# Optimization experiments

Hardware: AMD Instinct MI355X
Metric: run time of the kernel (lower is better)

## Reference

```python
import jax, jax.numpy as jnp
import numpy as np

EPS = 1e-05
B, M, N, P = 32, 1024, 1024, 256


def _xavier(key, shape):
    fan_in, fan_out = shape[0], shape[1]
    limit = np.sqrt(6.0 / (fan_in + fan_out))
    return jax.random.uniform(key, shape, jnp.float32, -limit, limit)


def setup_inputs() -> dict:
    key = jax.random.key(0)
    ks = jax.random.split(key, 6)
    return {
        "x": jax.random.normal(ks[0], (B, M, N), jnp.float32),
        "original_xj_y": _xavier(ks[1], (N, P)),
        "original_xi_y": _xavier(ks[2], (M, P)),
        "permuted_xj_y": _xavier(ks[3], (M, P)),
        "permuted_xi_y": _xavier(ks[4], (N, P)),
        "gamma_o_sum": jnp.ones((P,), jnp.float32),
        "gamma_o": jnp.ones((P, P), jnp.float32),
        "gamma_p_sum": jnp.ones((P,), jnp.float32),
        "gamma_p": jnp.ones((P, P), jnp.float32),
        "gamma": jnp.ones((P, P), jnp.float32),
        "beta_o_sum": jnp.zeros((P,), jnp.float32),
        "beta_o": jnp.zeros((P, P), jnp.float32),
        "beta_p_sum": jnp.zeros((P,), jnp.float32),
        "beta_p": jnp.zeros((P, P), jnp.float32),
        "beta": jnp.zeros((P, P), jnp.float32),
    }


def _normalize(x, axes, gamma, beta):
    mean = jnp.mean(x, axis=axes, keepdims=True)
    std = jnp.sqrt(jnp.var(x, axis=axes, keepdims=True, ddof=1))  # torch std is unbiased
    return gamma * ((x - mean) / (std + EPS)) + beta


def reference(x, original_xj_y, original_xi_y, permuted_xj_y, permuted_xi_y,
              gamma_o_sum, gamma_o, gamma_p_sum, gamma_p, gamma,
              beta_o_sum, beta_o, beta_p_sum, beta_p, beta):
    permuted = jnp.swapaxes(x, -1, -2)  # [B, N, M]

    # original path
    oyy = x @ original_xj_y                      # [B, M, P]
    o_sum = _normalize(oyy.sum(axis=-2), (-1,), gamma_o_sum, beta_o_sum) + 1.0  # [B, P]
    oyy = jnp.swapaxes(oyy, -1, -2) @ original_xi_y  # [B, P, P]
    oyy = jnp.swapaxes(oyy, -1, -2)
    oyy = _normalize(oyy, (-2, -1), gamma_o, beta_o)

    # permuted path
    pyy = permuted @ permuted_xj_y               # [B, N, P]
    p_sum = _normalize(pyy.sum(axis=-2), (-1,), gamma_p_sum, beta_p_sum) + 1.0  # [B, P]
    pyy = jnp.swapaxes(pyy, -1, -2) @ permuted_xi_y  # [B, P, P]
    pyy = jnp.swapaxes(pyy, -1, -2)
    pyy = _normalize(pyy, (-2, -1), gamma_p, beta_p)

    relations = jnp.einsum('ij,ik->ijk', o_sum, p_sum)  # [B, P, P]
    projected = (oyy * relations) @ (pyy * relations)   # [B, P, P]
    projected = _normalize(projected, (-2, -1), gamma, beta)
    return (projected, relations)
```

## Files before the change

### kernel.cpp

```cpp
#include <hip/hip_runtime.h>
#include <hip/hip_bf16.h>

#define PP 256
#define BB 32
#define MM 1024
#define NN 1024

constexpr float EPSF = 1e-5f;

typedef __attribute__((ext_vector_type(8))) short short8v;
typedef __attribute__((ext_vector_type(4))) short short4v;
typedef __attribute__((ext_vector_type(4))) float f32x4;

__device__ inline float bf2f(short s) {
  union { unsigned u; float f; } cv;
  cv.u = ((unsigned)(unsigned short)s) << 16;
  return cv.f;
}
__device__ inline short f2bf(float f) {
  union { float f; unsigned u; } cv; cv.f = f;
  unsigned u = cv.u;
  unsigned r = (u + 0x7fffu + ((u >> 16) & 1u)) >> 16;
  return (short)r;
}

__device__ inline void gload16(const void* g, void* l) {
  __builtin_amdgcn_global_load_lds(
      (const __attribute__((address_space(1))) unsigned*)g,
      (__attribute__((address_space(3))) unsigned*)l, 16, 0, 0);
}

__global__ __launch_bounds__(256)
void wconv4(const float* __restrict__ s0, const float* __restrict__ s1,
            const float* __restrict__ s2, const float* __restrict__ s3,
            short* __restrict__ d0, short* __restrict__ d1,
            short* __restrict__ d2, short* __restrict__ d3)
{
  const float* src = (blockIdx.z == 0) ? s0 : (blockIdx.z == 1) ? s1
                    : (blockIdx.z == 2) ? s2 : s3;
  short* dst = (blockIdx.z == 0) ? d0 : (blockIdx.z == 1) ? d1
              : (blockIdx.z == 2) ? d2 : d3;
  __shared__ float tile[64][65];
  const int c0 = blockIdx.x * 64, r0 = blockIdx.y * 64;
  const int tid = threadIdx.x;
#pragma unroll
  for (int i = 0; i < 16; ++i) {
    int idx = i * 256 + tid;
    int r = idx >> 6, c = idx & 63;
    tile[r][c] = src[(long)(r0 + r) * 256 + (c0 + c)];
  }
  __syncthreads();
#pragma unroll
  for (int i = 0; i < 16; ++i) {
    int idx = i * 256 + tid;
    int rr = idx >> 6, cc = idx & 63;
    dst[(long)(c0 + rr) * 1024 + (r0 + cc)] = f2bf(tile[cc][rr]);
  }
}

__global__ __launch_bounds__(256)
void tr2_f32(const float* __restrict__ s0, const float* __restrict__ s1,
             float* __restrict__ d0, float* __restrict__ d1)
{
  const float* src = blockIdx.z ? s1 : s0;
  float* dst = blockIdx.z ? d1 : d0;
  __shared__ float tile[64][65];
  const int c0 = blockIdx.x * 64, r0 = blockIdx.y * 64;
  const int tid = threadIdx.x;
#pragma unroll
  for (int i = 0; i < 16; ++i) {
    int idx = i * 256 + tid;
    int r = idx >> 6, c = idx & 63;
    tile[r][c] = src[(long)(r0 + r) * 256 + (c0 + c)];
  }
  __syncthreads();
#pragma unroll
  for (int i = 0; i < 16; ++i) {
    int idx = i * 256 + tid;
    int rr = idx >> 6, cc = idx & 63;
    dst[(long)(c0 + rr) * 256 + (r0 + cc)] = tile[cc][rr];
  }
}

__global__ __launch_bounds__(256, 4)
void gemm_xcat(const float* __restrict__ x, const short* __restrict__ wcat,
               short* __restrict__ oyyT, short* __restrict__ UT,
               float* __restrict__ rowsum)
{
  constexpr int BM = 128, BN = 128;
  __shared__ short As[2][4 * BM * 8];
  __shared__ short Bs[2][4 * BN * 8];

  const int b = blockIdx.z;
  const float* Ab = x + (long)b * MM * NN;
  const int m0 = blockIdx.x * BM;
  const int n0 = blockIdx.y * BN;

  const int tid = threadIdx.x;
  const int l = tid & 63, w = tid >> 6;
  const int wr = w >> 1, wc = w & 1;
  const int lk = l >> 4, lr = l & 15;
  const int sm = tid >> 2, skc = tid & 3;

  const float* aptr0 = Ab + (long)(m0 + sm) * NN + skc * 8;
  const float* aptr1 = Ab + (long)(m0 + 64 + sm) * NN + skc * 8;
  const int bn = tid & 127, bk0 = (tid >> 7) * 8;
  const short* bptr = wcat + (long)(n0 + bn) * NN + bk0;

  const int sA0 = ((skc * BM + sm) * 8) ^ (skc << 4);
  const int sA1 = ((skc * BM + 64 + sm) * 8) ^ (skc << 4);

  f32x4 acc[4][4];
#pragma unroll
  for (int fm = 0; fm < 4; ++fm)
#pragma unroll
    for (int fn = 0; fn < 4; ++fn)
      acc[fm][fn] = (f32x4){0.f, 0.f, 0.f, 0.f};

  float rs0 = 0.f, rs1 = 0.f;
  const bool doRs = (blockIdx.y == 0);
  float4 a00, a01, a10, a11;

#define XCAT_LOAD_A(k0_) do { \
    a00 = *reinterpret_cast<const float4*>(aptr0 + (k0_)); \
    a01 = *reinterpret_cast<const float4*>(aptr0 + (k0_) + 4); \
    a10 = *reinterpret_cast<const float4*>(aptr1 + (k0_)); \
    a11 = *reinterpret_cast<const float4*>(aptr1 + (k0_) + 4); \
  } while (0)

#define XCAT_STAGE_B(buf_, k0_) do { \
    gload16(bptr + (k0_), &Bs[buf_][tid * 8]); \
    gload16(bptr + (k0_) + 16, &Bs[buf_][(tid + 256) * 8]); \
  } while (0)

#define XCAT_STAGE_A(buf_) do { \
    if (doRs) { \
      rs0 += a00.x + a00.y + a00.z + a00.w + a01.x + a01.y + a01.z + a01.w; \
      rs1 += a10.x + a10.y + a10.z + a10.w + a11.x + a11.y + a11.z + a11.w; \
    } \
    short8v pk0, pk1; \
    pk0[0] = f2bf(a00.x); pk0[1] = f2bf(a00.y); pk0[2] = f2bf(a00.z); pk0[3] = f2bf(a00.w); \
    pk0[4] = f2bf(a01.x); pk0[5] = f2bf(a01.y); pk0[6] = f2bf(a01.z); pk0[7] = f2bf(a01.w); \
    pk1[0] = f2bf(a10.x); pk1[1] = f2bf(a10.y); pk1[2] = f2bf(a10.z); pk1[3] = f2bf(a10.w); \
    pk1[4] = f2bf(a11.x); pk1[5] = f2bf(a11.y); pk1[6] = f2bf(a11.z); pk1[7] = f2bf(a11.w); \
    *reinterpret_cast<short8v*>(&As[buf_][sA0]) = pk0; \
    *reinterpret_cast<short8v*>(&As[buf_][sA1]) = pk1; \
  } while (0)

  XCAT_LOAD_A(0);
  XCAT_STAGE_B(0, 0);
  XCAT_STAGE_A(0);
  __syncthreads();

  for (int kt = 0; kt < 32; ++kt) {
    const int cur = kt & 1, nxt = cur ^ 1;
    if (kt < 31) {
      const int k1 = (kt + 1) * 32;
      XCAT_LOAD_A(k1);
      XCAT_STAGE_B(nxt, k1);
    }
    short8v af[4], bf[4];
#pragma unroll
    for (int fm = 0; fm < 4; ++fm) {
      const int row = wr * 64 + fm * 16 + lr;
      af[fm] = *reinterpret_cast<const short8v*>(&As[cur][((lk * BM + row) * 8) ^ (lk << 4)]);
    }
#pragma unroll
    for (int fn = 0; fn < 4; ++fn)
      bf[fn] = *reinterpret_cast<const short8v*>(&Bs[cur][(lk * BN + wc * 64 + fn * 16 + lr) * 8]);
#pragma unroll
    for (int fm = 0; fm < 4; ++fm)
#pragma unroll
      for (int fn = 0; fn < 4; ++fn)
        acc[fm][fn] = __builtin_amdgcn_mfma_f32_16x16x32_bf16(
            af[fm], bf[fn], acc[fm][fn], 0, 0, 0);
    if (kt < 31) XCAT_STAGE_A(nxt);
    __syncthreads();
  }

  if (doRs) {
    rs0 += __shfl_xor(rs0, 1); rs0 += __shfl_xor(rs0, 2);
    rs1 += __shfl_xor(rs1, 1); rs1 += __shfl_xor(rs1, 2);
    if ((tid & 3) == 0) {
      rowsum[(long)b * MM + m0 + sm] = rs0;
      rowsum[(long)b * MM + m0 + 64 + sm] = rs1;
    }
  }

  short* Cb = ((n0 < 256) ? oyyT : UT) + (long)b * PP * MM;
  const int nb = n0 & 255;
#pragma unroll
  for (int fm = 0; fm < 4; ++fm)
#pragma unroll
    for (int fn = 0; fn < 4; ++fn) {
      const int c = nb + wc * 64 + fn * 16 + lr;
      const int rb = m0 + wr * 64 + fm * 16 + lk * 4;
      short4v pk;
#pragma unroll
      for (int j = 0; j < 4; ++j) pk[j] = f2bf(acc[fm][fn][j]);
      *reinterpret_cast<short4v*>(&Cb[(long)c * MM + rb]) = pk;
    }
}

__global__ __launch_bounds__(256)
void gemm_dual(const short* __restrict__ oyyT, const short* __restrict__ wo2T,
               const short* __restrict__ UT, const short* __restrict__ wp1T,
               float* __restrict__ t2T, float* __restrict__ p2)
{
  constexpr int BM = 64, BN = 64;
  __shared__ short As[2][4 * BM * 8];
  __shared__ short Bs[2][4 * BN * 8];

  const int z = blockIdx.z;
  const short* Ab; const short* Bb; float* Cb;
  if (z < 32) { Ab = oyyT + (long)z * PP * MM; Bb = wo2T; Cb = t2T + ((long)z << 16); }
  else { Ab = UT + (long)(z - 32) * PP * MM; Bb = wp1T; Cb = p2 + ((long)(z - 32) << 16); }

  const int m0 = blockIdx.x * BM, n0 = blockIdx.y * BN;
  const int tid = threadIdx.x;
  const int l = tid & 63, w = tid >> 6;
  const int wr = w >> 1, wc = w & 1;
  const int lk = l >> 4, lr = l & 15;
  const int kc = tid >> 6, mloc = tid & 63;
  const short* aP = Ab + (long)(m0 + mloc) * MM + kc * 8;
  const short* bP = Bb + (long)(n0 + mloc) * MM + kc * 8;

  f32x4 acc[2][2];
#pragma unroll
  for (int fm = 0; fm < 2; ++fm)
#pragma unroll
    for (int fn = 0; fn < 2; ++fn)
      acc[fm][fn] = (f32x4){0.f, 0.f, 0.f, 0.f};

  gload16(aP, &As[0][tid * 8]);
  gload16(bP, &Bs[0][tid * 8]);
  __syncthreads();

  for (int kt = 0; kt < 32; ++kt) {
    const int cur = kt & 1, nxt = cur ^ 1;
    if (kt < 31) {
      gload16(aP + (kt + 1) * 32, &As[nxt][tid * 8]);
      gload16(bP + (kt + 1) * 32, &Bs[nxt][tid * 8]);
    }
    short8v af[2], bf[2];
#pragma unroll
    for (int fm = 0; fm < 2; ++fm)
      af[fm] = *(const short8v*)&As[cur][(lk * BM + wr * 32 + fm * 16 + lr) * 8];
#pragma unroll
    for (int fn = 0; fn < 2; ++fn)
      bf[fn] = *(const short8v*)&Bs[cur][(lk * BN + wc * 32 + fn * 16 + lr) * 8];
#pragma unroll
    for (int fm = 0; fm < 2; ++fm)
#pragma unroll
      for (int fn = 0; fn < 2; ++fn)
        acc[fm][fn] = __builtin_amdgcn_mfma_f32_16x16x32_bf16(
            af[fm], bf[fn], acc[fm][fn], 0, 0, 0);
    __syncthreads();
  }

#pragma unroll
  for (int fm = 0; fm < 2; ++fm)
#pragma unroll
    for (int fn = 0; fn < 2; ++fn) {
      const int c = n0 + wc * 32 + fn * 16 + lr;
      const int rb = m0 + wr * 32 + fm * 16 + lk * 4;
      *(f32x4*)&Cb[(long)c * PP + rb] = acc[fm][fn];
    }
}

__global__ __launch_bounds__(256)
void gemm_pp(const short* __restrict__ A, const short* __restrict__ BT,
             float* __restrict__ C)
{
  constexpr int BM = 64, BN = 64;
  __shared__ short As[2][4 * BM * 8];
  __shared__ short Bs[2][4 * BN * 8];
  const int b = blockIdx.z;
  const short* Ab = A + ((long)b << 16);
  const short* Bb = BT + ((long)b << 16);
  float* Cb = C + ((long)b << 16);
  const int m0 = blockIdx.x * BM, n0 = blockIdx.y * BN;
  const int tid = threadIdx.x;
  const int l = tid & 63, w = tid >> 6;
  const int wr = w >> 1, wc = w & 1;
  const int lk = l >> 4, lr = l & 15;
  const int kc = tid >> 6, mloc = tid & 63;
  const short* aP = Ab + (long)(m0 + mloc) * PP + kc * 8;
  const short* bP = Bb + (long)(n0 + mloc) * PP + kc * 8;

  f32x4 acc[2][2];
#pragma unroll
  for (int fm = 0; fm < 2; ++fm)
#pragma unroll
    for (int fn = 0; fn < 2; ++fn)
      acc[fm][fn] = (f32x4){0.f, 0.f, 0.f, 0.f};

  gload16(aP, &As[0][tid * 8]);
  gload16(bP, &Bs[0][tid * 8]);
  __syncthreads();

  for (int kt = 0; kt < 8; ++kt) {
    const int cur = kt & 1, nxt = cur ^ 1;
    if (kt < 7) {
      gload16(aP + (kt + 1) * 32, &As[nxt][tid * 8]);
      gload16(bP + (kt + 1) * 32, &Bs[nxt][tid * 8]);
    }
    short8v af[2], bf[2];
#pragma unroll
    for (int fm = 0; fm < 2; ++fm)
      af[fm] = *(const short8v*)&As[cur][(lk * BM + wr * 32 + fm * 16 + lr) * 8];
#pragma unroll
    for (int fn = 0; fn < 2; ++fn)
      bf[fn] = *(const short8v*)&Bs[cur][(lk * BN + wc * 32 + fn * 16 + lr) * 8];
#pragma unroll
    for (int fm = 0; fm < 2; ++fm)
#pragma unroll
      for (int fn = 0; fn < 2; ++fn)
        acc[fm][fn] = __builtin_amdgcn_mfma_f32_16x16x32_bf16(
            af[fm], bf[fn], acc[fm][fn], 0, 0, 0);
    __syncthreads();
  }

#pragma unroll
  for (int fm = 0; fm < 2; ++fm)
#pragma unroll
    for (int fn = 0; fn < 2; ++fn) {
      const int c = n0 + wc * 32 + fn * 16 + lr;
      const int rb = m0 + wr * 32 + fm * 16 + lk * 4;
#pragma unroll
      for (int j = 0; j < 4; ++j)
        Cb[(long)(rb + j) * PP + c] = acc[fm][fn][j];
    }
}

__global__ __launch_bounds__(256)
void colsum_bf16(const short* __restrict__ srcT, float* __restrict__ raw)
{
  const int b = blockIdx.y;
  const int w = threadIdx.x >> 6, l = threadIdx.x & 63;
  const int p = blockIdx.x * 4 + w;
  const short* row = srcT + ((long)b * 256 + p) * 1024;
  short8v v1 = *(const short8v*)&row[l * 8];
  short8v v2 = *(const short8v*)&row[(64 + l) * 8];
  float s = 0.f;
#pragma unroll
  for (int j = 0; j < 8; ++j) s += bf2f(v1[j]) + bf2f(v2[j]);
#pragma unroll
  for (int off = 32; off; off >>= 1) s += __shfl_down(s, off);
  if (l == 0) raw[(long)b * 256 + p] = s;
}

__global__ __launch_bounds__(256)
void psum_dot(const short* __restrict__ wp1T, const float* __restrict__ rowsum,
              float* __restrict__ rawP)
{
  __shared__ float rsm[1024];
  const int b = blockIdx.x;
  for (int i = threadIdx.x; i < 1024; i += 256) rsm[i] = rowsum[(long)b * 1024 + i];
  __syncthreads();
  const int p = threadIdx.x;
  const short* wrow = wp1T + (long)p * 1024;
  float s = 0.f;
  for (int k = 0; k < 1024; k += 8) {
    short8v v = *(const short8v*)&wrow[k];
#pragma unroll
    for (int j = 0; j < 8; ++j) s = fmaf(bf2f(v[j]), rsm[k + j], s);
  }
  rawP[(long)b * 256 + p] = s;
}

__device__ inline void block_reduce2(float& v1, float& v2, float* red)
{
#pragma unroll
  for (int off = 32; off > 0; off >>= 1) {
    v1 += __shfl_down(v1, off);
    v2 += __shfl_down(v2, off);
  }
  const int lane = threadIdx.x & 63, wid = threadIdx.x >> 6;
  if (lane == 0) { red[wid * 2] = v1; red[wid * 2 + 1] = v2; }
  __syncthreads();
  v1 = red[0] + red[2] + red[4] + red[6];
  v2 = red[1] + red[3] + red[5] + red[7];
}

__global__ __launch_bounds__(256)
void norm_sum2(const float* __restrict__ raw2,
               const float* __restrict__ g_os, const float* __restrict__ b_os,
               const float* __restrict__ g_ps, const float* __restrict__ b_ps,
               float* __restrict__ o_sum, float* __restrict__ p_sum)
{
  const int bb = blockIdx.x;
  const bool isP = bb >= 32;
  const int b = bb & 31;
  const float* raw = raw2 + (isP ? 8192 : 0);
  const float* gamma = isP ? g_ps : g_os;
  const float* beta = isP ? b_ps : b_os;
  float* outp = isP ? p_sum : o_sum;
  const int p = threadIdx.x;
  float s = raw[(long)b * 256 + p];
  __shared__ float red[8];
  float v1 = s, v2 = s * s;
  block_reduce2(v1, v2, red);
  const float mean = v1 / 256.0f;
  float var = fmaxf((v2 - v1 * mean) / 255.0f, 0.f);
  const float inv = 1.0f / (sqrtf(var) + EPSF);
  outp[(long)b * 256 + p] = gamma[p] * (s - mean) * inv + beta[p] + 1.0f;
}

__global__ __launch_bounds__(256)
void stats_dual(const float* __restrict__ t2T, const float* __restrict__ p2,
                float* __restrict__ part)
{
  const int y = blockIdx.y, chunk = blockIdx.x;
  const float* s = (y < 32 ? t2T + ((long)y << 16)
                           : p2 + ((long)(y - 32) << 16)) + (long)chunk * 8192;
  float v1 = 0.f, v2 = 0.f;
  for (int i = threadIdx.x; i < 2048; i += 256) {
    float4 xv = *reinterpret_cast<const float4*>(&s[i * 4]);
    v1 += xv.x + xv.y + xv.z + xv.w;
    v2 = fmaf(xv.x, xv.x, fmaf(xv.y, xv.y, fmaf(xv.z, xv.z, fmaf(xv.w, xv.w, v2))));
  }
  __shared__ float red[8];
  block_reduce2(v1, v2, red);
  if (threadIdx.x == 0) {
    part[(y * 8 + chunk) * 2] = v1;
    part[(y * 8 + chunk) * 2 + 1] = v2;
  }
}

__global__ void stats_fin2(const float* __restrict__ part,
                           float* __restrict__ stO, float* __restrict__ stP)
{
  const int t = threadIdx.x;
  float v1 = 0.f, v2 = 0.f;
#pragma unroll
  for (int c = 0; c < 8; ++c) {
    v1 += part[(t * 8 + c) * 2];
    v2 += part[(t * 8 + c) * 2 + 1];
  }
  const float mean = v1 / 65536.0f;
  const float var = fmaxf((v2 - v1 * mean) / 65535.0f, 0.f);
  float* st = (t < 32) ? stO : stP;
  st[(t & 31) * 2] = mean;
  st[(t & 31) * 2 + 1] = 1.0f / (sqrtf(var) + EPSF);
}

__global__ __launch_bounds__(256)
void stats_part(const float* __restrict__ src, float* __restrict__ part)
{
  const int b = blockIdx.y, chunk = blockIdx.x;
  const float* s = src + ((long)b << 16) + (long)chunk * 8192;
  float v1 = 0.f, v2 = 0.f;
  for (int i = threadIdx.x; i < 2048; i += 256) {
    float4 xv = *reinterpret_cast<const float4*>(&s[i * 4]);
    v1 += xv.x + xv.y + xv.z + xv.w;
    v2 = fmaf(xv.x, xv.x, fmaf(xv.y, xv.y, fmaf(xv.z, xv.z, fmaf(xv.w, xv.w, v2))));
  }
  __shared__ float red[8];
  block_reduce2(v1, v2, red);
  if (threadIdx.x == 0) {
    part[(b * 8 + chunk) * 2] = v1;
    part[(b * 8 + chunk) * 2 + 1] = v2;
  }
}

__global__ void stats_fin(const float* __restrict__ part, float* __restrict__ st)
{
  const int b = threadIdx.x;
  if (b < 32) {
    float v1 = 0.f, v2 = 0.f;
#pragma unroll
    for (int c = 0; c < 8; ++c) {
      v1 += part[(b * 8 + c) * 2];
      v2 += part[(b * 8 + c) * 2 + 1];
    }
    const float mean = v1 / 65536.0f;
    const float var = fmaxf((v2 - v1 * mean) / 65535.0f, 0.f);
    st[b * 2] = mean;
    st[b * 2 + 1] = 1.0f / (sqrtf(var) + EPSF);
  }
}

__global__ __launch_bounds__(256)
void prep2(const float* __restrict__ t2T, const float* __restrict__ p2,
           const float* __restrict__ o_sum, const float* __restrict__ p_sum,
           const float* __restrict__ gamma_o, const float* __restrict__ beta_o,
           const float* __restrict__ gTp, const float* __restrict__ bTp,
           const float* __restrict__ stO, const float* __restrict__ stP,
           short* __restrict__ Ap, short* __restrict__ BpT,
           float* __restrict__ out)
{
  const long idx = (long)blockIdx.x * 256 + threadIdx.x;
  const int b = (int)(idx >> 16);
  const int rc = (int)(idx & 65535);
  const int r = rc >> 8, c = rc & 255;
  const float mO = stO[b * 2], iO = stO[b * 2 + 1];
  const float mP = stP[b * 2], iP = stP[b * 2 + 1];
  const float relA = o_sum[(b << 8) + r] * p_sum[(b << 8) + c];
  const float on = gamma_o[rc] * (t2T[idx] - mO) * iO + beta_o[rc];
  Ap[idx] = f2bf(on * relA);
  const float pn = gTp[rc] * (p2[idx] - mP) * iP + bTp[rc];
  BpT[idx] = f2bf(pn * o_sum[(b << 8) + c] * p_sum[(b << 8) + r]);
  out[(long)BB * 65536 + idx] = relA;
}

__global__ __launch_bounds__(256)
void final_half(const float* __restrict__ proj, const float* __restrict__ stF,
                const float* __restrict__ gamma, const float* __restrict__ beta,
                float* __restrict__ out)
{
  const long idx = (long)blockIdx.x * 256 + threadIdx.x;
  const int b = (int)(idx >> 16);
  const int ij = (int)(idx & 65535);
  out[idx] = gamma[ij] * (proj[idx] - stF[b * 2]) * stF[b * 2 + 1] + beta[ij];
}

extern "C" void kernel_launch(void* const* d_in, const int* in_sizes, int n_in,
                              void* d_out, int out_size, void* d_ws, size_t ws_size,
                              hipStream_t stream)
{
  const float* x    = (const float*)d_in[0];
  const float* Wo1  = (const float*)d_in[1];
  const float* Wo2  = (const float*)d_in[2];
  const float* Wp1  = (const float*)d_in[3];
  const float* Wp2  = (const float*)d_in[4];
  const float* g_os = (const float*)d_in[5];
  const float* g_o  = (const float*)d_in[6];
  const float* g_ps = (const float*)d_in[7];
  const float* g_p  = (const float*)d_in[8];
  const float* g    = (const float*)d_in[9];
  const float* b_os = (const float*)d_in[10];
  const float* b_o  = (const float*)d_in[11];
  const float* b_ps = (const float*)d_in[12];
  const float* b_p  = (const float*)d_in[13];
  const float* b_   = (const float*)d_in[14];
  float* out = (float*)d_out;

  short* wcat = (short*)d_ws;
  short* wo2T = wcat + 524288;
  short* wp1T = wo2T + 262144;
  short* oyyT = wp1T + 262144;
  short* UT   = oyyT + 8388608;
  float* gTp  = (float*)(UT + 8388608);
  float* bTp  = gTp + 65536;
  float* rowsumX = bTp + 65536;
  float* t2T  = rowsumX + 32768;
  float* p2   = t2T + 2097152;
  float* proj = p2 + 2097152;
  short* Ap   = (short*)(proj + 2097152);
  short* BpT  = Ap + 2097152;
  float* raw2 = (float*)(BpT + 2097152);
  float* o_sum = raw2 + 16384;
  float* p_sum = o_sum + 8192;
  float* part  = p_sum + 8192;
  float* partF = part + 1024;
  float* stO   = partF + 512;
  float* stP   = stO + 64;
  float* stF   = stP + 64;

  wconv4<<<dim3(4, 16, 4), 256, 0, stream>>>(Wo1, Wo2, Wp1, Wp2,
                                             wcat, wo2T, wp1T, wcat + 262144);
  tr2_f32<<<dim3(4, 4, 2), 256, 0, stream>>>(g_p, b_p, gTp, bTp);

  gemm_xcat<<<dim3(8, 4, 32), 256, 0, stream>>>(x, wcat, oyyT, UT, rowsumX);

  colsum_bf16<<<dim3(64, 32), 256, 0, stream>>>(oyyT, raw2);
  psum_dot<<<32, 256, 0, stream>>>(wp1T, rowsumX, raw2 + 8192);
  norm_sum2<<<64, 256, 0, stream>>>(raw2, g_os, b_os, g_ps, b_ps, o_sum, p_sum);

  gemm_dual<<<dim3(4, 4, 64), 256, 0, stream>>>(oyyT, wo2T, UT, wp1T, t2T, p2);

  stats_dual<<<dim3(8, 64), 256, 0, stream>>>(t2T, p2, part);
  stats_fin2<<<1, 64, 0, stream>>>(part, stO, stP);

  prep2<<<8192, 256, 0, stream>>>(t2T, p2, o_sum, p_sum, g_o, b_o, gTp, bTp,
                                  stO, stP, Ap, BpT, out);

  gemm_pp<<<dim3(4, 4, 32), 256, 0, stream>>>(Ap, BpT, proj);

  stats_part<<<dim3(8, 32), 256, 0, stream>>>(proj, partF);
  stats_fin<<<1, 64, 0, stream>>>(partF, stF);

  final_half<<<8192, 256, 0, stream>>>(proj, stF, g, b_, out);
}
```

Baseline: 168.9 us.

## Triple-buffer B tiles and remap gemm_xcat blocks for XCD locality

The main x-projection GEMM now uses a 1D grid, with a block-index remap that spreads consecutive hardware IDs across the 8 XCDs so blocks sharing the same x rows sit together. The B operand gets a three-stage LDS ring prefetched two iterations ahead. A manual vmcnt wait plus raw barrier replaces __syncthreads so one B load can stay in flight. The occupancy hint in launch_bounds is dropped, and the extra LDS buffer may lower occupancy. gemm_dual and gemm_pp are only moved within the file.

New measurement: 191.8 us. 13.5% more time.

```diff
diff --git a/kernel.cpp b/kernel.cpp
--- a/kernel.cpp
+++ b/kernel.cpp
@@ -82,19 +82,23 @@
   }
 }
 
-__global__ __launch_bounds__(256, 4)
+__global__ __launch_bounds__(256)
 void gemm_xcat(const float* __restrict__ x, const short* __restrict__ wcat,
                short* __restrict__ oyyT, short* __restrict__ UT,
                float* __restrict__ rowsum)
 {
-  constexpr int BM = 128, BN = 128;
-  __shared__ short As[2][4 * BM * 8];
-  __shared__ short Bs[2][4 * BN * 8];
-
-  const int b = blockIdx.z;
+  __shared__ short As[2][4096];
+  __shared__ short Bs[3][4096];
+
+  const int hwid = blockIdx.x;
+  const int work = (hwid & 7) * 128 + (hwid >> 3);
+  const int nblk = work & 3;
+  const int mblk = (work >> 2) & 7;
+  const int b    = work >> 5;
+
   const float* Ab = x + (long)b * MM * NN;
-  const int m0 = blockIdx.x * BM;
-  const int n0 = blockIdx.y * BN;
+  const int m0 = mblk * 128;
+  const int n0 = nblk * 128;
 
   const int tid = threadIdx.x;
   const int l = tid & 63, w = tid >> 6;
@@ -103,12 +107,15 @@
   const int sm = tid >> 2, skc = tid & 3;
 
   const float* aptr0 = Ab + (long)(m0 + sm) * NN + skc * 8;
-  const float* aptr1 = Ab + (long)(m0 + 64 + sm) * NN + skc * 8;
-  const int bn = tid & 127, bk0 = (tid >> 7) * 8;
-  const short* bptr = wcat + (long)(n0 + bn) * NN + bk0;
-
-  const int sA0 = ((skc * BM + sm) * 8) ^ (skc << 4);
-  const int sA1 = ((skc * BM + 64 + sm) * 8) ^ (skc << 4);
+  const float* aptr1 = aptr0 + 64 * NN;
+  const int sA0 = ((skc * 128 + sm) * 8) ^ (skc << 4);
+  const int sA1 = ((skc * 128 + 64 + sm) * 8) ^ (skc << 4);
+
+  const int bn0 = tid & 127, bkc0 = tid >> 7;
+  const int bn1 = bn0, bkc1 = bkc0 + 2;
+  const short* bptrA = wcat + (long)(n0 + bn0) * NN + bkc0 * 8;
+  const short* bptrB = wcat + (long)(n0 + bn1) * NN + bkc1 * 8;
+  const int sBA = tid * 8, sBB = (tid + 256) * 8;
 
   f32x4 acc[4][4];
 #pragma unroll
@@ -118,22 +125,22 @@
       acc[fm][fn] = (f32x4){0.f, 0.f, 0.f, 0.f};
 
   float rs0 = 0.f, rs1 = 0.f;
-  const bool doRs = (blockIdx.y == 0);
+  const bool doRs = (nblk == 0);
   float4 a00, a01, a10, a11;
 
-#define XCAT_LOAD_A(k0_) do { \
+#define XC_LOAD_A(k0_) do { \
     a00 = *reinterpret_cast<const float4*>(aptr0 + (k0_)); \
     a01 = *reinterpret_cast<const float4*>(aptr0 + (k0_) + 4); \
     a10 = *reinterpret_cast<const float4*>(aptr1 + (k0_)); \
     a11 = *reinterpret_cast<const float4*>(aptr1 + (k0_) + 4); \
   } while (0)
 
-#define XCAT_STAGE_B(buf_, k0_) do { \
-    gload16(bptr + (k0_), &Bs[buf_][tid * 8]); \
-    gload16(bptr + (k0_) + 16, &Bs[buf_][(tid + 256) * 8]); \
+#define XC_STAGE_B(buf_, k0_) do { \
+    gload16(bptrA + (k0_), &Bs[buf_][sBA]); \
+    gload16(bptrB + (k0_), &Bs[buf_][sBB]); \
   } while (0)
 
-#define XCAT_STAGE_A(buf_) do { \
+#define XC_STAGE_A(buf_) do { \
     if (doRs) { \
       rs0 += a00.x + a00.y + a00.z + a00.w + a01.x + a01.y + a01.z + a01.w; \
       rs1 += a10.x + a10.y + a10.z + a10.w + a11.x + a11.y + a11.z + a11.w; \
@@ -147,41 +154,51 @@
     *reinterpret_cast<short8v*>(&As[buf_][sA1]) = pk1; \
   } while (0)
 
-  XCAT_LOAD_A(0);
-  XCAT_STAGE_B(0, 0);
-  XCAT_STAGE_A(0);
-  __syncthreads();
-
+  XC_LOAD_A(0);
+  XC_STAGE_B(0, 0);
+  XC_STAGE_B(1, 32);
+  XC_STAGE_A(0);
+  asm volatile("s_waitcnt vmcnt(2) lgkmcnt(0)" ::: "memory");
+  __builtin_amdgcn_s_barrier();
+  __builtin_amdgcn_sched_barrier(0);
+
+  int curB = 0, nxtB = 2;
+  int curA = 0;
   for (int kt = 0; kt < 32; ++kt) {
-    const int cur = kt & 1, nxt = cur ^ 1;
-    if (kt < 31) {
-      const int k1 = (kt + 1) * 32;
-      XCAT_LOAD_A(k1);
-      XCAT_STAGE_B(nxt, k1);
-    }
+    if (kt < 31) XC_LOAD_A((kt + 1) * 32);
+    if (kt < 30) XC_STAGE_B(nxtB, (kt + 2) * 32);
+
     short8v af[4], bf[4];
 #pragma unroll
     for (int fm = 0; fm < 4; ++fm) {
       const int row = wr * 64 + fm * 16 + lr;
-      af[fm] = *reinterpret_cast<const short8v*>(&As[cur][((lk * BM + row) * 8) ^ (lk << 4)]);
+      af[fm] = *reinterpret_cast<const short8v*>(
+          &As[curA][((lk * 128 + row) * 8) ^ (lk << 4)]);
     }
 #pragma unroll
     for (int fn = 0; fn < 4; ++fn)
-      bf[fn] = *reinterpret_cast<const short8v*>(&Bs[cur][(lk * BN + wc * 64 + fn * 16 + lr) * 8]);
+      bf[fn] = *reinterpret_cast<const short8v*>(
+          &Bs[curB][(lk * 128 + wc * 64 + fn * 16 + lr) * 8]);
 #pragma unroll
     for (int fm = 0; fm < 4; ++fm)
 #pragma unroll
       for (int fn = 0; fn < 4; ++fn)
         acc[fm][fn] = __builtin_amdgcn_mfma_f32_16x16x32_bf16(
             af[fm], bf[fn], acc[fm][fn], 0, 0, 0);
-    if (kt < 31) XCAT_STAGE_A(nxt);
-    __syncthreads();
+
+    if (kt < 31) XC_STAGE_A(curA ^ 1);
+    asm volatile("s_waitcnt vmcnt(2) lgkmcnt(0)" ::: "memory");
+    __builtin_amdgcn_s_barrier();
+    __builtin_amdgcn_sched_barrier(0);
+    curA ^= 1;
+    curB = (curB == 2) ? 0 : curB + 1;
+    nxtB = (nxtB == 2) ? 0 : nxtB + 1;
   }
 
   if (doRs) {
     rs0 += __shfl_xor(rs0, 1); rs0 += __shfl_xor(rs0, 2);
     rs1 += __shfl_xor(rs1, 1); rs1 += __shfl_xor(rs1, 2);
-    if ((tid & 3) == 0) {
+    if (skc == 0) {
       rowsum[(long)b * MM + m0 + sm] = rs0;
       rowsum[(long)b * MM + m0 + 64 + sm] = rs1;
     }
@@ -199,137 +216,6 @@
 #pragma unroll
       for (int j = 0; j < 4; ++j) pk[j] = f2bf(acc[fm][fn][j]);
       *reinterpret_cast<short4v*>(&Cb[(long)c * MM + rb]) = pk;
-    }
-}
-
-__global__ __launch_bounds__(256)
-void gemm_dual(const short* __restrict__ oyyT, const short* __restrict__ wo2T,
-               const short* __restrict__ UT, const short* __restrict__ wp1T,
-               float* __restrict__ t2T, float* __restrict__ p2)
-{
-  constexpr int BM = 64, BN = 64;
-  __shared__ short As[2][4 * BM * 8];
-  __shared__ short Bs[2][4 * BN * 8];
-
-  const int z = blockIdx.z;
-  const short* Ab; const short* Bb; float* Cb;
-  if (z < 32) { Ab = oyyT + (long)z * PP * MM; Bb = wo2T; Cb = t2T + ((long)z << 16); }
-  else { Ab = UT + (long)(z - 32) * PP * MM; Bb = wp1T; Cb = p2 + ((long)(z - 32) << 16); }
-
-  const int m0 = blockIdx.x * BM, n0 = blockIdx.y * BN;
-  const int tid = threadIdx.x;
-  const int l = tid & 63, w = tid >> 6;
-  const int wr = w >> 1, wc = w & 1;
-  const int lk = l >> 4, lr = l & 15;
-  const int kc = tid >> 6, mloc = tid & 63;
-  const short* aP = Ab + (long)(m0 + mloc) * MM + kc * 8;
-  const short* bP = Bb + (long)(n0 + mloc) * MM + kc * 8;
-
-  f32x4 acc[2][2];
-#pragma unroll
-  for (int fm = 0; fm < 2; ++fm)
-#pragma unroll
-    for (int fn = 0; fn < 2; ++fn)
-      acc[fm][fn] = (f32x4){0.f, 0.f, 0.f, 0.f};
-
-  gload16(aP, &As[0][tid * 8]);
-  gload16(bP, &Bs[0][tid * 8]);
-  __syncthreads();
-
-  for (int kt = 0; kt < 32; ++kt) {
-    const int cur = kt & 1, nxt = cur ^ 1;
-    if (kt < 31) {
-      gload16(aP + (kt + 1) * 32, &As[nxt][tid * 8]);
-      gload16(bP + (kt + 1) * 32, &Bs[nxt][tid * 8]);
-    }
-    short8v af[2], bf[2];
-#pragma unroll
-    for (int fm = 0; fm < 2; ++fm)
-      af[fm] = *(const short8v*)&As[cur][(lk * BM + wr * 32 + fm * 16 + lr) * 8];
-#pragma unroll
-    for (int fn = 0; fn < 2; ++fn)
-      bf[fn] = *(const short8v*)&Bs[cur][(lk * BN + wc * 32 + fn * 16 + lr) * 8];
-#pragma unroll
-    for (int fm = 0; fm < 2; ++fm)
-#pragma unroll
-      for (int fn = 0; fn < 2; ++fn)
-        acc[fm][fn] = __builtin_amdgcn_mfma_f32_16x16x32_bf16(
-            af[fm], bf[fn], acc[fm][fn], 0, 0, 0);
-    __syncthreads();
-  }
-
-#pragma unroll
-  for (int fm = 0; fm < 2; ++fm)
-#pragma unroll
-    for (int fn = 0; fn < 2; ++fn) {
-      const int c = n0 + wc * 32 + fn * 16 + lr;
-      const int rb = m0 + wr * 32 + fm * 16 + lk * 4;
-      *(f32x4*)&Cb[(long)c * PP + rb] = acc[fm][fn];
-    }
-}
-
-__global__ __launch_bounds__(256)
-void gemm_pp(const short* __restrict__ A, const short* __restrict__ BT,
-             float* __restrict__ C)
-{
-  constexpr int BM = 64, BN = 64;
-  __shared__ short As[2][4 * BM * 8];
-  __shared__ short Bs[2][4 * BN * 8];
-  const int b = blockIdx.z;
-  const short* Ab = A + ((long)b << 16);
-  const short* Bb = BT + ((long)b << 16);
-  float* Cb = C + ((long)b << 16);
-  const int m0 = blockIdx.x * BM, n0 = blockIdx.y * BN;
-  const int tid = threadIdx.x;
-  const int l = tid & 63, w = tid >> 6;
-  const int wr = w >> 1, wc = w & 1;
-  const int lk = l >> 4, lr = l & 15;
-  const int kc = tid >> 6, mloc = tid & 63;
-  const short* aP = Ab + (long)(m0 + mloc) * PP + kc * 8;
-  const short* bP = Bb + (long)(n0 + mloc) * PP + kc * 8;
-
-  f32x4 acc[2][2];
-#pragma unroll
-  for (int fm = 0; fm < 2; ++fm)
-#pragma unroll
-    for (int fn = 0; fn < 2; ++fn)
-      acc[fm][fn] = (f32x4){0.f, 0.f, 0.f, 0.f};
-
-  gload16(aP, &As[0][tid * 8]);
-  gload16(bP, &Bs[0][tid * 8]);
-  __syncthreads();
-
-  for (int kt = 0; kt < 8; ++kt) {
-    const int cur = kt & 1, nxt = cur ^ 1;
-    if (kt < 7) {
-      gload16(aP + (kt + 1) * 32, &As[nxt][tid * 8]);
-      gload16(bP + (kt + 1) * 32, &Bs[nxt][tid * 8]);
-    }
-    short8v af[2], bf[2];
-#pragma unroll
-    for (int fm = 0; fm < 2; ++fm)
-      af[fm] = *(const short8v*)&As[cur][(lk * BM + wr * 32 + fm * 16 + lr) * 8];
-#pragma unroll
-    for (int fn = 0; fn < 2; ++fn)
-      bf[fn] = *(const short8v*)&Bs[cur][(lk * BN + wc * 32 + fn * 16 + lr) * 8];
-#pragma unroll
-    for (int fm = 0; fm < 2; ++fm)
-#pragma unroll
-      for (int fn = 0; fn < 2; ++fn)
-        acc[fm][fn] = __builtin_amdgcn_mfma_f32_16x16x32_bf16(
-            af[fm], bf[fn], acc[fm][fn], 0, 0, 0);
-    __syncthreads();
-  }
-
-#pragma unroll
-  for (int fm = 0; fm < 2; ++fm)
-#pragma unroll
-    for (int fn = 0; fn < 2; ++fn) {
-      const int c = n0 + wc * 32 + fn * 16 + lr;
-      const int rb = m0 + wr * 32 + fm * 16 + lk * 4;
-#pragma unroll
-      for (int j = 0; j < 4; ++j)
-        Cb[(long)(rb + j) * PP + c] = acc[fm][fn][j];
     }
 }
 
@@ -405,6 +291,137 @@
   float var = fmaxf((v2 - v1 * mean) / 255.0f, 0.f);
   const float inv = 1.0f / (sqrtf(var) + EPSF);
   outp[(long)b * 256 + p] = gamma[p] * (s - mean) * inv + beta[p] + 1.0f;
+}
+
+__global__ __launch_bounds__(256)
+void gemm_dual(const short* __restrict__ oyyT, const short* __restrict__ wo2T,
+               const short* __restrict__ UT, const short* __restrict__ wp1T,
+               float* __restrict__ t2T, float* __restrict__ p2)
+{
+  constexpr int BM = 64, BN = 64;
+  __shared__ short As[2][4 * BM * 8];
+  __shared__ short Bs[2][4 * BN * 8];
+
+  const int z = blockIdx.z;
+  const short* Ab; const short* Bb; float* Cb;
+  if (z < 32) { Ab = oyyT + (long)z * PP * MM; Bb = wo2T; Cb = t2T + ((long)z << 16); }
+  else { Ab = UT + (long)(z - 32) * PP * MM; Bb = wp1T; Cb = p2 + ((long)(z - 32) << 16); }
+
+  const int m0 = blockIdx.x * BM, n0 = blockIdx.y * BN;
+  const int tid = threadIdx.x;
+  const int l = tid & 63, w = tid >> 6;
+  const int wr = w >> 1, wc = w & 1;
+  const int lk = l >> 4, lr = l & 15;
+  const int kc = tid >> 6, mloc = tid & 63;
+  const short* aP = Ab + (long)(m0 + mloc) * MM + kc * 8;
+  const short* bP = Bb + (long)(n0 + mloc) * MM + kc * 8;
+
+  f32x4 acc[2][2];
+#pragma unroll
+  for (int fm = 0; fm < 2; ++fm)
+#pragma unroll
+    for (int fn = 0; fn < 2; ++fn)
+      acc[fm][fn] = (f32x4){0.f, 0.f, 0.f, 0.f};
+
+  gload16(aP, &As[0][tid * 8]);
+  gload16(bP, &Bs[0][tid * 8]);
+  __syncthreads();
+
+  for (int kt = 0; kt < 32; ++kt) {
+    const int cur = kt & 1, nxt = cur ^ 1;
+    if (kt < 31) {
+      gload16(aP + (kt + 1) * 32, &As[nxt][tid * 8]);
+      gload16(bP + (kt + 1) * 32, &Bs[nxt][tid * 8]);
+    }
+    short8v af[2], bf[2];
+#pragma unroll
+    for (int fm = 0; fm < 2; ++fm)
+      af[fm] = *(const short8v*)&As[cur][(lk * BM + wr * 32 + fm * 16 + lr) * 8];
+#pragma unroll
+    for (int fn = 0; fn < 2; ++fn)
+      bf[fn] = *(const short8v*)&Bs[cur][(lk * BN + wc * 32 + fn * 16 + lr) * 8];
+#pragma unroll
+    for (int fm = 0; fm < 2; ++fm)
+#pragma unroll
+      for (int fn = 0; fn < 2; ++fn)
+        acc[fm][fn] = __builtin_amdgcn_mfma_f32_16x16x32_bf16(
+            af[fm], bf[fn], acc[fm][fn], 0, 0, 0);
+    __syncthreads();
+  }
+
+#pragma unroll
+  for (int fm = 0; fm < 2; ++fm)
+#pragma unroll
+    for (int fn = 0; fn < 2; ++fn) {
+      const int c = n0 + wc * 32 + fn * 16 + lr;
+      const int rb = m0 + wr * 32 + fm * 16 + lk * 4;
+      *(f32x4*)&Cb[(long)c * PP + rb] = acc[fm][fn];
+    }
+}
+
+__global__ __launch_bounds__(256)
+void gemm_pp(const short* __restrict__ A, const short* __restrict__ BT,
+             float* __restrict__ C)
+{
+  constexpr int BM = 64, BN = 64;
+  __shared__ short As[2][4 * BM * 8];
+  __shared__ short Bs[2][4 * BN * 8];
+  const int b = blockIdx.z;
+  const short* Ab = A + ((long)b << 16);
+  const short* Bb = BT + ((long)b << 16);
+  float* Cb = C + ((long)b << 16);
+  const int m0 = blockIdx.x * BM, n0 = blockIdx.y * BN;
+  const int tid = threadIdx.x;
+  const int l = tid & 63, w = tid >> 6;
+  const int wr = w >> 1, wc = w & 1;
+  const int lk = l >> 4, lr = l & 15;
+  const int kc = tid >> 6, mloc = tid & 63;
+  const short* aP = Ab + (long)(m0 + mloc) * PP + kc * 8;
+  const short* bP = Bb + (long)(n0 + mloc) * PP + kc * 8;
+
+  f32x4 acc[2][2];
+#pragma unroll
+  for (int fm = 0; fm < 2; ++fm)
+#pragma unroll
+    for (int fn = 0; fn < 2; ++fn)
+      acc[fm][fn] = (f32x4){0.f, 0.f, 0.f, 0.f};
+
+  gload16(aP, &As[0][tid * 8]);
+  gload16(bP, &Bs[0][tid * 8]);
+  __syncthreads();
+
+  for (int kt = 0; kt < 8; ++kt) {
+    const int cur = kt & 1, nxt = cur ^ 1;
+    if (kt < 7) {
+      gload16(aP + (kt + 1) * 32, &As[nxt][tid * 8]);
+      gload16(bP + (kt + 1) * 32, &Bs[nxt][tid * 8]);
+    }
+    short8v af[2], bf[2];
+#pragma unroll
+    for (int fm = 0; fm < 2; ++fm)
+      af[fm] = *(const short8v*)&As[cur][(lk * BM + wr * 32 + fm * 16 + lr) * 8];
+#pragma unroll
+    for (int fn = 0; fn < 2; ++fn)
+      bf[fn] = *(const short8v*)&Bs[cur][(lk * BN + wc * 32 + fn * 16 + lr) * 8];
+#pragma unroll
+    for (int fm = 0; fm < 2; ++fm)
+#pragma unroll
+      for (int fn = 0; fn < 2; ++fn)
+        acc[fm][fn] = __builtin_amdgcn_mfma_f32_16x16x32_bf16(
+            af[fm], bf[fn], acc[fm][fn], 0, 0, 0);
+    __syncthreads();
+  }
+
+#pragma unroll
+  for (int fm = 0; fm < 2; ++fm)
+#pragma unroll
+    for (int fn = 0; fn < 2; ++fn) {
+      const int c = n0 + wc * 32 + fn * 16 + lr;
+      const int rb = m0 + wr * 32 + fm * 16 + lk * 4;
+#pragma unroll
+      for (int j = 0; j < 4; ++j)
+        Cb[(long)(rb + j) * PP + c] = acc[fm][fn][j];
+    }
 }
 
 __global__ __launch_bounds__(256)
@@ -562,7 +579,7 @@
                                              wcat, wo2T, wp1T, wcat + 262144);
   tr2_f32<<<dim3(4, 4, 2), 256, 0, stream>>>(g_p, b_p, gTp, bTp);
 
-  gemm_xcat<<<dim3(8, 4, 32), 256, 0, stream>>>(x, wcat, oyyT, UT, rowsumX);
+  gemm_xcat<<<dim3(1024, 1, 1), 256, 0, stream>>>(x, wcat, oyyT, UT, rowsumX);
 
   colsum_bf16<<<dim3(64, 32), 256, 0, stream>>>(oyyT, raw2);
   psum_dot<<<32, 256, 0, stream>>>(wp1T, rowsumX, raw2 + 8192);
```
